# Optimization experiments

Measured on AMD Instinct MI355X. Metric: run time of the kernel, lower is better.

The kernel has to match this reference:

```python
import jax, jax.numpy as jnp
import numpy as np

K = 3       # kernel size
PAD = 1     # k // 2
S = 1       # stride
EPS = 1e-5  # BatchNorm eps


def setup_inputs() -> dict:
    key = jax.random.key(0)
    ks = jax.random.split(key, 7)
    B, C1, C2, H, W = 4, 256, 256, 80, 80
    x = jax.random.normal(ks[0], (B, C1, H, W), dtype=jnp.float32)
    # offset/mask conv params (orig inits these to zero; use small random so
    # the deformable sampling path is actually exercised)
    w_off = jax.random.normal(ks[1], (3 * K * K, C1, K, K), dtype=jnp.float32) * 0.01
    b_off = jax.random.normal(ks[2], (3 * K * K,), dtype=jnp.float32) * 0.01
    weight = jax.random.normal(ks[3], (C2, C1, K, K), dtype=jnp.float32) * 0.05
    bias = jax.random.normal(ks[4], (C2,), dtype=jnp.float32) * 0.05
    gamma = jnp.ones((C2,), dtype=jnp.float32)
    beta = jnp.zeros((C2,), dtype=jnp.float32)
    return {"x": x, "w_off": w_off, "b_off": b_off, "weight": weight,
            "bias": bias, "gamma": gamma, "beta": beta}


def _elastic_head(x, w_off, b_off, weight, bias, gamma, beta):
    B, C, H, W = x.shape
    K2 = K * K
    # offset/mask predictor conv (stride 1, SAME padding -> output H x W)
    off_out = jax.lax.conv_general_dilated(
        x, w_off, (S, S), 'SAME',
        dimension_numbers=('NCHW', 'OIHW', 'NCHW')) + b_off[None, :, None, None]
    o1, o2, m = off_out[:, :K2], off_out[:, K2:2 * K2], off_out[:, 2 * K2:]
    mask = jax.nn.sigmoid(m)                                   # [B,K2,H,W]
    # torchvision layout: channel 2p = dy_p, 2p+1 = dx_p
    off = jnp.concatenate([o1, o2], axis=1).reshape(B, K2, 2, H, W)
    dy, dx = off[:, :, 0], off[:, :, 1]                        # [B,K2,H,W]
    # base sampling grid per kernel tap
    ii, jj = jnp.meshgrid(jnp.arange(K), jnp.arange(K), indexing='ij')
    ii = ii.reshape(K2)
    jj = jj.reshape(K2)
    base_y = (jnp.arange(H)[None, :] * S - PAD + ii[:, None]).astype(x.dtype)  # [K2,H]
    base_x = (jnp.arange(W)[None, :] * S - PAD + jj[:, None]).astype(x.dtype)  # [K2,W]
    ys = dy + base_y[None, :, :, None]                         # [B,K2,H,W]
    xs = dx + base_x[None, :, None, :]
    y0 = jnp.floor(ys)
    x0 = jnp.floor(xs)
    wy = ys - y0
    wx = xs - x0
    y0i = y0.astype(jnp.int32)
    x0i = x0.astype(jnp.int32)
    y1i = y0i + 1
    x1i = x0i + 1
    x_flat = x.reshape(B, C, H * W)

    def gather(yy, xx):
        valid = ((yy >= 0) & (yy < H) & (xx >= 0) & (xx < W)).astype(x.dtype)
        idx = jnp.clip(yy, 0, H - 1) * W + jnp.clip(xx, 0, W - 1)
        g = jax.vmap(lambda xf, ix: xf[:, ix])(x_flat, idx.reshape(B, -1))
        return g.reshape(B, C, K2, H, W) * valid[:, None]

    # bilinear sample with zero padding outside, accumulate corners
    patches = (gather(y0i, x0i) * ((1 - wy) * (1 - wx))[:, None]
               + gather(y0i, x1i) * ((1 - wy) * wx)[:, None]
               + gather(y1i, x0i) * (wy * (1 - wx))[:, None]
               + gather(y1i, x1i) * (wy * wx)[:, None])       # [B,C,K2,H,W]
    patches = patches * mask[:, None]                          # modulation
    # implicit GEMM of deform_conv2d
    out = jnp.einsum('bcphw,ocp->bohw', patches,
                     weight.reshape(weight.shape[0], C, K2)) + bias[None, :, None, None]
    # BatchNorm2d (training-mode batch stats, biased variance) + SiLU
    mean = out.mean(axis=(0, 2, 3))
    var = out.var(axis=(0, 2, 3))
    xn = (out - mean[None, :, None, None]) * jax.lax.rsqrt(var + EPS)[None, :, None, None]
    y_bn = xn * gamma[None, :, None, None] + beta[None, :, None, None]
    return y_bn * jax.nn.sigmoid(y_bn)


def reference(x, w_off, b_off, weight, bias, gamma, beta):
    return _elastic_head(x, w_off, b_off, weight, bias, gamma, beta)
```

## Files before the change

### kernel.cpp

```cpp
#include <hip/hip_runtime.h>
#include <math.h>

constexpr int Hc = 80, Wc = 80, Bn = 4, C1 = 256, C2 = 256;
constexpr int HWn = Hc * Wc;
constexpr int NPIX = Bn * HWn;
constexpr int OFFC = 27;
constexpr int KK   = 2304;

typedef short bf16x8 __attribute__((ext_vector_type(8)));
typedef float f32x4  __attribute__((ext_vector_type(4)));

__device__ __forceinline__ unsigned f2bf(float f) {
    unsigned u = __float_as_uint(f);
    return (u + 0x7FFF + ((u >> 16) & 1)) >> 16;
}

__device__ __forceinline__ unsigned packhi2(float v0, float v1) {
    unsigned h;
    asm("v_cvt_pk_bf16_f32 %0, %1, %2" : "=v"(h) : "v"(v0), "v"(v1));
    return h;
}

__global__ __launch_bounds__(256) void k_wprep(const float* __restrict__ weight,
                                               unsigned short* __restrict__ wB1)
{
    int e = blockIdx.x * 256 + threadIdx.x;
    int kc = e % 40;
    int oc = (e / 40) & 255;
    int s  = e / 10240;
    int p  = s >> 3, cc = s & 7;
    float w = 0.f;
    if (kc < 32) w = weight[((size_t)oc * C1 + cc * 32 + kc) * 9 + p];
    wB1[e] = (unsigned short)f2bf(w);
}

__global__ __launch_bounds__(256) void k_wobprep(const float* __restrict__ w_off,
                                                 unsigned short* __restrict__ wOB)
{
    int e = blockIdx.x * 256 + threadIdx.x;
    int k  = e & 31;
    int oc = (e >> 5) & 31;
    int s  = e >> 10;
    int p  = s >> 3, cc = s & 7;
    float v = 0.f;
    if (oc < 27) v = w_off[((size_t)oc * C1 + cc * 32 + k) * 9 + p];
    wOB[e] = (unsigned short)f2bf(v);
}

__global__ __launch_bounds__(256) void k_xtrans(const float* __restrict__ x,
                                                float* __restrict__ xT,
                                                unsigned short* __restrict__ xTb)
{
    __shared__ float tile[32][33];
    int bid = blockIdx.x;
    int ct  = bid & 7;
    int hwt = (bid >> 3) % 200;
    int b   = bid / 1600;
    int c0  = ct * 32, hw0 = hwt * 32;
    int tid = threadIdx.x;
    int col = tid & 31, rw = tid >> 5;
    const float* xb = x + (size_t)b * C1 * HWn;
    #pragma unroll
    for (int k = 0; k < 4; ++k) {
        int r = rw + k * 8;
        tile[r][col] = xb[(size_t)(c0 + r) * HWn + hw0 + col];
    }
    __syncthreads();
    float* xo = xT + ((size_t)b * HWn + hw0) * C1 + c0;
    unsigned short* xob = xTb + ((size_t)b * HWn + hw0) * C1 + c0;
    #pragma unroll
    for (int k = 0; k < 4; ++k) {
        int r = rw + k * 8;
        float v = tile[col][r];
        xo[(size_t)r * C1 + col]  = v;
        xob[(size_t)r * C1 + col] = (unsigned short)f2bf(v);
    }
}

__global__ __launch_bounds__(256) void k_offmfma(const unsigned short* __restrict__ xTb,
                                                 const unsigned short* __restrict__ wOB,
                                                 const float* __restrict__ b_off,
                                                 float* __restrict__ off)
{
    int t  = threadIdx.x;
    int wv = t >> 6, lane = t & 63;
    int li = lane & 15, kg = lane >> 4;
    int mi = wv & 1;
    int nj = wv >> 1;

    int mtile = ((blockIdx.x & 7) * 100) + (blockIdx.x >> 3);
    int m0  = mtile * 32;
    int b   = m0 / HWn;
    int hw0 = m0 - b * HWn;
    int pxl = hw0 + mi * 16 + li;
    int h = pxl / Wc, w = pxl - h * Wc;

    const unsigned short* xb = xTb + (size_t)b * HWn * C1;

    f32x4 acc = (f32x4){0.f, 0.f, 0.f, 0.f};
    #pragma unroll
    for (int p = 0; p < 9; ++p) {
        int dh = p / 3 - 1, dw = p % 3 - 1;
        int hh = h + dh, ww = w + dw;
        bool valid = (hh >= 0 && hh < Hc && ww >= 0 && ww < Wc);
        int hwp = valid ? (hh * Wc + ww) : 0;
        const unsigned short* arow = xb + (size_t)hwp * C1 + kg * 8;
        const unsigned short* brow = wOB + ((size_t)(p * 8) * 32 + nj * 16 + li) * 32 + kg * 8;
        #pragma unroll
        for (int cc = 0; cc < 8; ++cc) {
            uint4 av = *(const uint4*)(arow + cc * 32);
            if (!valid) av = make_uint4(0, 0, 0, 0);
            uint4 bv = *(const uint4*)(brow + cc * 1024);
            acc = __builtin_amdgcn_mfma_f32_16x16x32_bf16(
                __builtin_bit_cast(bf16x8, av), __builtin_bit_cast(bf16x8, bv), acc, 0, 0, 0);
        }
    }
    int oc = nj * 16 + li;
    if (oc < OFFC) {
        float bs = b_off[oc];
        float4 v;
        v.x = acc[0] + bs; v.y = acc[1] + bs; v.z = acc[2] + bs; v.w = acc[3] + bs;
        int hwd = hw0 + mi * 16 + kg * 4;
        *(float4*)&off[((size_t)b * OFFC + oc) * HWn + hwd] = v;
    }
}

__global__ __launch_bounds__(256) void k_meta(const float* __restrict__ off,
                                              int* __restrict__ crdbuf,
                                              float4* __restrict__ w4buf)
{
    int pair = blockIdx.x * 256 + threadIdx.x;
    int px = pair / 9, p = pair - px * 9;
    int b  = px / HWn, hw = px - b * HWn;
    int h = hw / Wc, w = hw - h * Wc;
    int ii = p / 3, jj = p - ii * 3;

    const float* ob = off + (size_t)b * OFFC * HWn + hw;
    float dy = ob[(2 * p) * HWn];
    float dx = ob[(2 * p + 1) * HWn];
    float mv = ob[(18 + p) * HWn];
    float mask = 1.0f / (1.0f + expf(-mv));
    float ys = dy + (float)(h - 1 + ii);
    float xsv = dx + (float)(w - 1 + jj);
    float y0f = floorf(ys), x0f = floorf(xsv);
    float wy = ys - y0f, wx = xsv - x0f;
    int y0 = (int)y0f, x0 = (int)x0f;
    int y1 = y0 + 1, x1 = x0 + 1;
    float vy0 = (y0 >= 0 && y0 < Hc) ? 1.f : 0.f;
    float vy1 = (y1 >= 0 && y1 < Hc) ? 1.f : 0.f;
    float vx0 = (x0 >= 0 && x0 < Wc) ? 1.f : 0.f;
    float vx1 = (x1 >= 0 && x1 < Wc) ? 1.f : 0.f;
    float4 wv;
    wv.x = mask * (1.f - wy) * (1.f - wx) * vy0 * vx0;
    wv.y = mask * (1.f - wy) * wx         * vy0 * vx1;
    wv.z = mask * wy         * (1.f - wx) * vy1 * vx0;
    wv.w = mask * wy         * wx         * vy1 * vx1;
    int cy0 = min(max(y0, 0), Hc - 1), cy1 = min(max(y1, 0), Hc - 1);
    int cx0 = min(max(x0, 0), Wc - 1), cx1 = min(max(x1, 0), Wc - 1);
    crdbuf[pair] = cy0 | (cy1 << 8) | (cx0 << 16) | (cx1 << 24);
    w4buf[pair]  = wv;
}

__global__ __launch_bounds__(256) void k_gather(const float* __restrict__ xT,
                                                const int* __restrict__ crdbuf,
                                                const float4* __restrict__ w4buf,
                                                unsigned short* __restrict__ Ahi)
{
    int t   = threadIdx.x;
    int wv  = t >> 6, l = t & 63;
    int xcd = blockIdx.x & 7;
    int blk = blockIdx.x >> 3;
    int wgl = (xcd * 100 + blk) * 4 + wv;
    int base = wgl * 72;

    #pragma unroll 2
    for (int i = 0; i < 72; ++i) {
        int pair = base + i;
        int px = pair / 9, p = pair - px * 9;
        int b  = px / HWn;
        int crd = crdbuf[pair];
        float4 w4 = w4buf[pair];
        int cy0 = crd & 255, cy1 = (crd >> 8) & 255;
        int cx0 = (crd >> 16) & 255, cx1 = (crd >> 24) & 255;
        const float* xt = xT + (size_t)b * HWn * C1;
        const float4* g00p = (const float4*)&xt[(size_t)(cy0 * Wc + cx0) * C1];
        const float4* g01p = (const float4*)&xt[(size_t)(cy0 * Wc + cx1) * C1];
        const float4* g10p = (const float4*)&xt[(size_t)(cy1 * Wc + cx0) * C1];
        const float4* g11p = (const float4*)&xt[(size_t)(cy1 * Wc + cx1) * C1];
        float4 g00 = g00p[l], g01 = g01p[l], g10 = g10p[l], g11 = g11p[l];
        float vx = fmaf(w4.x, g00.x, fmaf(w4.y, g01.x, fmaf(w4.z, g10.x, w4.w * g11.x)));
        float vy = fmaf(w4.x, g00.y, fmaf(w4.y, g01.y, fmaf(w4.z, g10.y, w4.w * g11.y)));
        float vz = fmaf(w4.x, g00.z, fmaf(w4.y, g01.z, fmaf(w4.z, g10.z, w4.w * g11.z)));
        float vw = fmaf(w4.x, g00.w, fmaf(w4.y, g01.w, fmaf(w4.z, g10.w, w4.w * g11.w)));
        unsigned h0 = packhi2(vx, vy), h1 = packhi2(vz, vw);
        int s = p * 8 + (l >> 3);
        size_t aidx = ((size_t)s * NPIX + px) * 32 + 4 * (l & 7);
        *(uint2*)&Ahi[aidx] = make_uint2(h0, h1);
    }
}

__global__ __launch_bounds__(256, 4) void k_dmfma(const unsigned short* __restrict__ Ahi,
                                                  const unsigned short* __restrict__ wB1,
                                                  const float* __restrict__ bias,
                                                  float* __restrict__ out)
{
    __shared__ __align__(16) char smem[40960];
    float* Tb = (float*)smem;

    int t  = threadIdx.x;
    int wv = t >> 6, lane = t & 63;
    int li = lane & 15, kg = lane >> 4;
    int mi = wv & 1;
    int nh = wv >> 1;

    int mtile = ((blockIdx.x & 7) * 100) + (blockIdx.x >> 3);
    int m0  = mtile * 32;
    int b   = m0 / HWn;
    int hw0 = m0 - b * HWn;
    int row = m0 + mi * 16 + li;

    auto gllB = [&](int s, int buf) {
        const char* src = (const char*)wB1 + (size_t)s * 20480 + wv * 5120 + lane * 16;
        char* dst = smem + buf * 20480 + wv * 5120;
        #pragma unroll
        for (int i = 0; i < 5; ++i)
            __builtin_amdgcn_global_load_lds(
                (const __attribute__((address_space(1))) void*)(src + i * 1024),
                (__attribute__((address_space(3))) void*)(dst + i * 1024),
                16, 0, 0);
    };
    auto loadA = [&](int s, uint4& hh) {
        size_t base = ((size_t)s * NPIX + row) * 32 + kg * 8;
        hh = *(const uint4*)(Ahi + base);
    };

    f32x4 acc[8];
    #pragma unroll
    for (int n = 0; n < 8; ++n) acc[n] = (f32x4){0.f, 0.f, 0.f, 0.f};

    uint4 a0h, a1h, a2h;
    loadA(0, a0h);
    gllB(0, 0);
    loadA(1, a1h);

    auto step = [&](int s, uint4& ch, uint4& lh) {
        if (s == 71) { asm volatile("s_waitcnt vmcnt(0)" ::: "memory"); }
        else         { asm volatile("s_waitcnt vmcnt(1)" ::: "memory"); }
        __builtin_amdgcn_s_barrier();
        __builtin_amdgcn_sched_barrier(0);
        int cur = s & 1;
        if (s < 71) gllB(s + 1, cur ^ 1);
        __builtin_amdgcn_sched_barrier(0);
        if (s < 70) loadA(s + 2, lh);
        __builtin_amdgcn_sched_barrier(0);
        const unsigned short* Bc = (const unsigned short*)(smem + cur * 20480);
        bf16x8 ah = __builtin_bit_cast(bf16x8, ch);
        __builtin_amdgcn_s_setprio(1);
        #pragma unroll
        for (int nt = 0; nt < 8; ++nt) {
            int oc = nh * 128 + nt * 16 + li;
            bf16x8 bv = *(const bf16x8*)&Bc[oc * 40 + kg * 8];
            acc[nt] = __builtin_amdgcn_mfma_f32_16x16x32_bf16(ah, bv, acc[nt], 0, 0, 0);
        }
        __builtin_amdgcn_s_setprio(0);
    };

    for (int s = 0; s < 72; s += 3) {
        step(s,     a0h, a2h);
        step(s + 1, a1h, a0h);
        step(s + 2, a2h, a1h);
    }

    #pragma unroll
    for (int q = 0; q < 8; ++q) {
        __syncthreads();
        if (nh == (q >> 2)) {
            #pragma unroll
            for (int j = 0; j < 2; ++j) {
                int nt = (q & 3) * 2 + j;
                f32x4 a = acc[nt];
                int rrw = j * 16 + li;
                int col = mi * 16 + kg * 4;
                #pragma unroll
                for (int r = 0; r < 4; ++r)
                    Tb[rrw * 33 + col + r] = a[r];
            }
        }
        __syncthreads();
        int px = t & 31;
        int rw = t >> 5;
        #pragma unroll
        for (int it = 0; it < 4; ++it) {
            int r  = it * 8 + rw;
            int oc = q * 32 + r;
            out[(size_t)(b * C2 + oc) * HWn + hw0 + px] = Tb[r * 33 + px] + bias[oc];
        }
    }
}

__global__ __launch_bounds__(256) void k_bnstats(const float* __restrict__ out,
                                                 float* __restrict__ stats)
{
    int oc = blockIdx.x;
    double s = 0.0, ss = 0.0;
    for (int i = threadIdx.x; i < NPIX; i += 256) {
        int bb = i / HWn;
        int hw = i - bb * HWn;
        float v = out[(size_t)(bb * C2 + oc) * HWn + hw];
        s  += (double)v;
        ss += (double)v * (double)v;
    }
    __shared__ double ls[256], lss[256];
    ls[threadIdx.x] = s; lss[threadIdx.x] = ss;
    __syncthreads();
    for (int st = 128; st > 0; st >>= 1) {
        if (threadIdx.x < st) {
            ls[threadIdx.x]  += ls[threadIdx.x + st];
            lss[threadIdx.x] += lss[threadIdx.x + st];
        }
        __syncthreads();
    }
    if (threadIdx.x == 0) {
        double mean = ls[0] / (double)NPIX;
        double var  = lss[0] / (double)NPIX - mean * mean;
        stats[oc]       = (float)mean;
        stats[256 + oc] = (float)(1.0 / sqrt(var + 1e-5));
    }
}

__global__ __launch_bounds__(256) void k_bnsilu(float* __restrict__ out,
                                                const float* __restrict__ stats,
                                                const float* __restrict__ gamma,
                                                const float* __restrict__ beta)
{
    int n4 = (Bn * C2 * HWn) / 4;
    for (int i = blockIdx.x * blockDim.x + threadIdx.x; i < n4;
         i += gridDim.x * blockDim.x) {
        float4 v = ((float4*)out)[i];
        int e  = i * 4;
        int oc = (e / HWn) & 255;
        float mean = stats[oc];
        float gs   = gamma[oc] * stats[256 + oc];
        float bt   = beta[oc];
        float y;
        y = (v.x - mean) * gs + bt; v.x = y / (1.f + expf(-y));
        y = (v.y - mean) * gs + bt; v.y = y / (1.f + expf(-y));
        y = (v.z - mean) * gs + bt; v.z = y / (1.f + expf(-y));
        y = (v.w - mean) * gs + bt; v.w = y / (1.f + expf(-y));
        ((float4*)out)[i] = v;
    }
}

extern "C" void kernel_launch(void* const* d_in, const int* in_sizes, int n_in,
                              void* d_out, int out_size, void* d_ws, size_t ws_size,
                              hipStream_t stream)
{
    const float* x      = (const float*)d_in[0];
    const float* w_off  = (const float*)d_in[1];
    const float* b_off  = (const float*)d_in[2];
    const float* weight = (const float*)d_in[3];
    const float* bias   = (const float*)d_in[4];
    const float* gamma  = (const float*)d_in[5];
    const float* beta   = (const float*)d_in[6];
    float* out = (float*)d_out;

    char* wsb = (char*)d_ws;
    unsigned short* Ahi  = (unsigned short*)(wsb);
    float*          xT   = (float*)(wsb + 117964800);
    unsigned short* xTb  = (unsigned short*)(wsb + 144179200);
    float*          off  = (float*)(wsb + 157286400);
    unsigned short* wB1  = (unsigned short*)(wsb + 160051200);
    unsigned short* wOB  = (unsigned short*)(wsb + 161525760);
    int*            crdb = (int*)(wsb + 161673216);
    float4*         w4b  = (float4*)(wsb + 162594816);
    float*         stats = (float*)(wsb + 166281216);

    k_wprep    <<<2880, 256, 0, stream>>>(weight, wB1);
    k_wobprep  <<<288, 256, 0, stream>>>(w_off, wOB);
    k_xtrans   <<<6400, 256, 0, stream>>>(x, xT, xTb);
    k_offmfma  <<<800, 256, 0, stream>>>(xTb, wOB, b_off, off);
    k_meta     <<<900, 256, 0, stream>>>(off, crdb, w4b);
    k_gather   <<<800, 256, 0, stream>>>(xT, crdb, w4b, Ahi);
    k_dmfma    <<<800, 256, 0, stream>>>(Ahi, wB1, bias, out);
    k_bnstats  <<<256, 256, 0, stream>>>(out, stats);
    k_bnsilu   <<<2048, 256, 0, stream>>>(out, stats, gamma, beta);
}
```

Before: 250.7 us.

## Retile deform GEMM waves to 2x4 MFMA blocks with unpadded kg-major B layout

Each wave in the main deformable-conv GEMM now computes both 16-row M halves over 64 output channels, instead of one M half over 128 channels. Each B fragment read from LDS now feeds two MFMAs, and each wave issues two A loads per step. The weight prep kernel writes B in a kg-major layout without the 40-element padding, so each K-step's B slice shrinks from 20 KB to 16 KB and LDS use drops. The unpadded layout may cause LDS bank conflicts, and the extra in-flight global loads change the vmcnt accounting.

```diff
diff --git a/kernel.cpp b/kernel.cpp
--- a/kernel.cpp
+++ b/kernel.cpp
@@ -25,12 +25,12 @@
                                                unsigned short* __restrict__ wB1)
 {
     int e = blockIdx.x * 256 + threadIdx.x;
-    int kc = e % 40;
-    int oc = (e / 40) & 255;
-    int s  = e / 10240;
-    int p  = s >> 3, cc = s & 7;
-    float w = 0.f;
-    if (kc < 32) w = weight[((size_t)oc * C1 + cc * 32 + kc) * 9 + p];
+    int kin = e & 7;
+    int oc  = (e >> 3) & 255;
+    int kg  = (e >> 11) & 3;
+    int s   = e >> 13;
+    int p   = s >> 3, cc = s & 7;
+    float w = weight[((size_t)oc * C1 + cc * 32 + kg * 8 + kin) * 9 + p];
     wB1[e] = (unsigned short)f2bf(w);
 }
 
@@ -204,86 +204,93 @@
                                                   const float* __restrict__ bias,
                                                   float* __restrict__ out)
 {
-    __shared__ __align__(16) char smem[40960];
+    __shared__ __align__(16) char smem[32768];
     float* Tb = (float*)smem;
 
     int t  = threadIdx.x;
     int wv = t >> 6, lane = t & 63;
     int li = lane & 15, kg = lane >> 4;
-    int mi = wv & 1;
-    int nh = wv >> 1;
+    int nh = wv;
 
     int mtile = ((blockIdx.x & 7) * 100) + (blockIdx.x >> 3);
     int m0  = mtile * 32;
     int b   = m0 / HWn;
     int hw0 = m0 - b * HWn;
-    int row = m0 + mi * 16 + li;
+    int row0 = m0 + li;
+    int row1 = m0 + 16 + li;
 
     auto gllB = [&](int s, int buf) {
-        const char* src = (const char*)wB1 + (size_t)s * 20480 + wv * 5120 + lane * 16;
-        char* dst = smem + buf * 20480 + wv * 5120;
-        #pragma unroll
-        for (int i = 0; i < 5; ++i)
+        const char* src = (const char*)wB1 + (size_t)s * 16384 + t * 16;
+        char* dst = smem + buf * 16384 + t * 16;
+        #pragma unroll
+        for (int i = 0; i < 4; ++i)
             __builtin_amdgcn_global_load_lds(
-                (const __attribute__((address_space(1))) void*)(src + i * 1024),
-                (__attribute__((address_space(3))) void*)(dst + i * 1024),
+                (const __attribute__((address_space(1))) void*)(src + i * 4096),
+                (__attribute__((address_space(3))) void*)(dst + i * 4096),
                 16, 0, 0);
     };
-    auto loadA = [&](int s, uint4& hh) {
-        size_t base = ((size_t)s * NPIX + row) * 32 + kg * 8;
-        hh = *(const uint4*)(Ahi + base);
+    auto loadA = [&](int s, uint4& h0, uint4& h1) {
+        size_t base = (size_t)s * NPIX * 32 + (size_t)kg * 8;
+        h0 = *(const uint4*)(Ahi + base + (size_t)row0 * 32);
+        h1 = *(const uint4*)(Ahi + base + (size_t)row1 * 32);
     };
 
-    f32x4 acc[8];
-    #pragma unroll
-    for (int n = 0; n < 8; ++n) acc[n] = (f32x4){0.f, 0.f, 0.f, 0.f};
-
-    uint4 a0h, a1h, a2h;
-    loadA(0, a0h);
+    f32x4 acc[2][4];
+    #pragma unroll
+    for (int m = 0; m < 2; ++m)
+        #pragma unroll
+        for (int n = 0; n < 4; ++n) acc[m][n] = (f32x4){0.f, 0.f, 0.f, 0.f};
+
+    uint4 a0m0, a0m1, a1m0, a1m1, a2m0, a2m1;
+    loadA(0, a0m0, a0m1);
     gllB(0, 0);
-    loadA(1, a1h);
-
-    auto step = [&](int s, uint4& ch, uint4& lh) {
+    loadA(1, a1m0, a1m1);
+
+    auto step = [&](int s, uint4& c0, uint4& c1, uint4& l0, uint4& l1) {
         if (s == 71) { asm volatile("s_waitcnt vmcnt(0)" ::: "memory"); }
-        else         { asm volatile("s_waitcnt vmcnt(1)" ::: "memory"); }
+        else         { asm volatile("s_waitcnt vmcnt(2)" ::: "memory"); }
         __builtin_amdgcn_s_barrier();
         __builtin_amdgcn_sched_barrier(0);
         int cur = s & 1;
         if (s < 71) gllB(s + 1, cur ^ 1);
         __builtin_amdgcn_sched_barrier(0);
-        if (s < 70) loadA(s + 2, lh);
+        if (s < 70) loadA(s + 2, l0, l1);
         __builtin_amdgcn_sched_barrier(0);
-        const unsigned short* Bc = (const unsigned short*)(smem + cur * 20480);
-        bf16x8 ah = __builtin_bit_cast(bf16x8, ch);
+        const unsigned short* Bc = (const unsigned short*)(smem + cur * 16384);
+        bf16x8 a0 = __builtin_bit_cast(bf16x8, c0);
+        bf16x8 a1 = __builtin_bit_cast(bf16x8, c1);
         __builtin_amdgcn_s_setprio(1);
         #pragma unroll
-        for (int nt = 0; nt < 8; ++nt) {
-            int oc = nh * 128 + nt * 16 + li;
-            bf16x8 bv = *(const bf16x8*)&Bc[oc * 40 + kg * 8];
-            acc[nt] = __builtin_amdgcn_mfma_f32_16x16x32_bf16(ah, bv, acc[nt], 0, 0, 0);
+        for (int nt = 0; nt < 4; ++nt) {
+            bf16x8 bv = *(const bf16x8*)&Bc[(kg * 256 + nh * 64 + nt * 16 + li) * 8];
+            acc[0][nt] = __builtin_amdgcn_mfma_f32_16x16x32_bf16(a0, bv, acc[0][nt], 0, 0, 0);
+            acc[1][nt] = __builtin_amdgcn_mfma_f32_16x16x32_bf16(a1, bv, acc[1][nt], 0, 0, 0);
         }
         __builtin_amdgcn_s_setprio(0);
     };
 
     for (int s = 0; s < 72; s += 3) {
-        step(s,     a0h, a2h);
-        step(s + 1, a1h, a0h);
-        step(s + 2, a2h, a1h);
+        step(s,     a0m0, a0m1, a2m0, a2m1);
+        step(s + 1, a1m0, a1m1, a0m0, a0m1);
+        step(s + 2, a2m0, a2m1, a1m0, a1m1);
     }
 
     #pragma unroll
     for (int q = 0; q < 8; ++q) {
         __syncthreads();
-        if (nh == (q >> 2)) {
+        if (nh == (q >> 1)) {
             #pragma unroll
-            for (int j = 0; j < 2; ++j) {
-                int nt = (q & 3) * 2 + j;
-                f32x4 a = acc[nt];
-                int rrw = j * 16 + li;
-                int col = mi * 16 + kg * 4;
+            for (int jj = 0; jj < 2; ++jj) {
+                int nt = (q & 1) * 2 + jj;
                 #pragma unroll
-                for (int r = 0; r < 4; ++r)
-                    Tb[rrw * 33 + col + r] = a[r];
+                for (int m = 0; m < 2; ++m) {
+                    f32x4 a = acc[m][nt];
+                    int rrw = jj * 16 + li;
+                    int col = m * 16 + kg * 4;
+                    #pragma unroll
+                    for (int r = 0; r < 4; ++r)
+                        Tb[rrw * 33 + col + r] = a[r];
+                }
             }
         }
         __syncthreads();
@@ -370,12 +377,12 @@
     unsigned short* xTb  = (unsigned short*)(wsb + 144179200);
     float*          off  = (float*)(wsb + 157286400);
     unsigned short* wB1  = (unsigned short*)(wsb + 160051200);
-    unsigned short* wOB  = (unsigned short*)(wsb + 161525760);
-    int*            crdb = (int*)(wsb + 161673216);
-    float4*         w4b  = (float4*)(wsb + 162594816);
-    float*         stats = (float*)(wsb + 166281216);
-
-    k_wprep    <<<2880, 256, 0, stream>>>(weight, wB1);
+    unsigned short* wOB  = (unsigned short*)(wsb + 161230848);
+    int*            crdb = (int*)(wsb + 161378304);
+    float4*         w4b  = (float4*)(wsb + 162299904);
+    float*         stats = (float*)(wsb + 165986304);
+
+    k_wprep    <<<2304, 256, 0, stream>>>(weight, wB1);
     k_wobprep  <<<288, 256, 0, stream>>>(w_off, wOB);
     k_xtrans   <<<6400, 256, 0, stream>>>(x, xT, xTb);
     k_offmfma  <<<800, 256, 0, stream>>>(xTb, wOB, b_off, off);
```

Measured after the change: 253.0 us. Within noise of the previous version (+0.9%).

## Fuse bilinear gather into deformable-conv MFMA kernel, drop im2col buffer

Applied to the files above, without the earlier changes.

Merges the gather kernel and the MFMA GEMM kernel. Each wave now computes its bilinearly sampled bf16 A-fragments in registers straight from xT, so the ~118 MB im2col buffer Ahi is never written to or read back from HBM. Weights are repacked into a layout the MFMA B operand can load directly from global memory, which replaces the double-buffered LDS staging and barriers. In exchange, every block issues scattered gathers with no software pipelining, and B-fragment loads now come from L2 rather than LDS, so latency may be exposed and there may be less overlap with the matrix work.

```diff
diff --git a/kernel.cpp b/kernel.cpp
--- a/kernel.cpp
+++ b/kernel.cpp
@@ -25,12 +25,12 @@
                                                unsigned short* __restrict__ wB1)
 {
     int e = blockIdx.x * 256 + threadIdx.x;
-    int kc = e % 40;
-    int oc = (e / 40) & 255;
-    int s  = e / 10240;
-    int p  = s >> 3, cc = s & 7;
-    float w = 0.f;
-    if (kc < 32) w = weight[((size_t)oc * C1 + cc * 32 + kc) * 9 + p];
+    int kin = e & 7;
+    int oc  = (e >> 3) & 255;
+    int kg  = (e >> 11) & 3;
+    int s   = e >> 13;
+    int p   = s >> 3, cc = s & 7;
+    float w = weight[((size_t)oc * C1 + cc * 32 + kg * 8 + kin) * 9 + p];
     wB1[e] = (unsigned short)f2bf(w);
 }
 
@@ -161,51 +161,14 @@
     w4buf[pair]  = wv;
 }
 
-__global__ __launch_bounds__(256) void k_gather(const float* __restrict__ xT,
+__global__ __launch_bounds__(256) void k_dfused(const float* __restrict__ xT,
                                                 const int* __restrict__ crdbuf,
                                                 const float4* __restrict__ w4buf,
-                                                unsigned short* __restrict__ Ahi)
-{
-    int t   = threadIdx.x;
-    int wv  = t >> 6, l = t & 63;
-    int xcd = blockIdx.x & 7;
-    int blk = blockIdx.x >> 3;
-    int wgl = (xcd * 100 + blk) * 4 + wv;
-    int base = wgl * 72;
-
-    #pragma unroll 2
-    for (int i = 0; i < 72; ++i) {
-        int pair = base + i;
-        int px = pair / 9, p = pair - px * 9;
-        int b  = px / HWn;
-        int crd = crdbuf[pair];
-        float4 w4 = w4buf[pair];
-        int cy0 = crd & 255, cy1 = (crd >> 8) & 255;
-        int cx0 = (crd >> 16) & 255, cx1 = (crd >> 24) & 255;
-        const float* xt = xT + (size_t)b * HWn * C1;
-        const float4* g00p = (const float4*)&xt[(size_t)(cy0 * Wc + cx0) * C1];
-        const float4* g01p = (const float4*)&xt[(size_t)(cy0 * Wc + cx1) * C1];
-        const float4* g10p = (const float4*)&xt[(size_t)(cy1 * Wc + cx0) * C1];
-        const float4* g11p = (const float4*)&xt[(size_t)(cy1 * Wc + cx1) * C1];
-        float4 g00 = g00p[l], g01 = g01p[l], g10 = g10p[l], g11 = g11p[l];
-        float vx = fmaf(w4.x, g00.x, fmaf(w4.y, g01.x, fmaf(w4.z, g10.x, w4.w * g11.x)));
-        float vy = fmaf(w4.x, g00.y, fmaf(w4.y, g01.y, fmaf(w4.z, g10.y, w4.w * g11.y)));
-        float vz = fmaf(w4.x, g00.z, fmaf(w4.y, g01.z, fmaf(w4.z, g10.z, w4.w * g11.z)));
-        float vw = fmaf(w4.x, g00.w, fmaf(w4.y, g01.w, fmaf(w4.z, g10.w, w4.w * g11.w)));
-        unsigned h0 = packhi2(vx, vy), h1 = packhi2(vz, vw);
-        int s = p * 8 + (l >> 3);
-        size_t aidx = ((size_t)s * NPIX + px) * 32 + 4 * (l & 7);
-        *(uint2*)&Ahi[aidx] = make_uint2(h0, h1);
-    }
-}
-
-__global__ __launch_bounds__(256, 4) void k_dmfma(const unsigned short* __restrict__ Ahi,
-                                                  const unsigned short* __restrict__ wB1,
-                                                  const float* __restrict__ bias,
-                                                  float* __restrict__ out)
-{
-    __shared__ __align__(16) char smem[40960];
-    float* Tb = (float*)smem;
+                                                const unsigned short* __restrict__ wB1,
+                                                const float* __restrict__ bias,
+                                                float* __restrict__ out)
+{
+    __shared__ float Tb[32 * 33];
 
     int t  = threadIdx.x;
     int wv = t >> 6, lane = t & 63;
@@ -217,58 +180,57 @@
     int m0  = mtile * 32;
     int b   = m0 / HWn;
     int hw0 = m0 - b * HWn;
-    int row = m0 + mi * 16 + li;
-
-    auto gllB = [&](int s, int buf) {
-        const char* src = (const char*)wB1 + (size_t)s * 20480 + wv * 5120 + lane * 16;
-        char* dst = smem + buf * 20480 + wv * 5120;
+    int px  = m0 + mi * 16 + li;
+
+    const float* xtb = xT + (size_t)b * HWn * C1;
+
+    f32x4 acc[8];
+    #pragma unroll
+    for (int n = 0; n < 8; ++n) acc[n] = (f32x4){0.f, 0.f, 0.f, 0.f};
+
+    #pragma unroll 1
+    for (int p = 0; p < 9; ++p) {
+        int pair = px * 9 + p;
+        int crd = crdbuf[pair];
+        float4 w4 = w4buf[pair];
+        int cy0 = crd & 255, cy1 = (crd >> 8) & 255;
+        int cx0 = (crd >> 16) & 255, cx1 = (crd >> 24) & 255;
+        const float* c00 = &xtb[(size_t)(cy0 * Wc + cx0) * C1 + kg * 8];
+        const float* c01 = &xtb[(size_t)(cy0 * Wc + cx1) * C1 + kg * 8];
+        const float* c10 = &xtb[(size_t)(cy1 * Wc + cx0) * C1 + kg * 8];
+        const float* c11 = &xtb[(size_t)(cy1 * Wc + cx1) * C1 + kg * 8];
         #pragma unroll
-        for (int i = 0; i < 5; ++i)
-            __builtin_amdgcn_global_load_lds(
-                (const __attribute__((address_space(1))) void*)(src + i * 1024),
-                (__attribute__((address_space(3))) void*)(dst + i * 1024),
-                16, 0, 0);
-    };
-    auto loadA = [&](int s, uint4& hh) {
-        size_t base = ((size_t)s * NPIX + row) * 32 + kg * 8;
-        hh = *(const uint4*)(Ahi + base);
-    };
-
-    f32x4 acc[8];
-    #pragma unroll
-    for (int n = 0; n < 8; ++n) acc[n] = (f32x4){0.f, 0.f, 0.f, 0.f};
-
-    uint4 a0h, a1h, a2h;
-    loadA(0, a0h);
-    gllB(0, 0);
-    loadA(1, a1h);
-
-    auto step = [&](int s, uint4& ch, uint4& lh) {
-        if (s == 71) { asm volatile("s_waitcnt vmcnt(0)" ::: "memory"); }
-        else         { asm volatile("s_waitcnt vmcnt(1)" ::: "memory"); }
-        __builtin_amdgcn_s_barrier();
-        __builtin_amdgcn_sched_barrier(0);
-        int cur = s & 1;
-        if (s < 71) gllB(s + 1, cur ^ 1);
-        __builtin_amdgcn_sched_barrier(0);
-        if (s < 70) loadA(s + 2, lh);
-        __builtin_amdgcn_sched_barrier(0);
-        const unsigned short* Bc = (const unsigned short*)(smem + cur * 20480);
-        bf16x8 ah = __builtin_bit_cast(bf16x8, ch);
-        __builtin_amdgcn_s_setprio(1);
-        #pragma unroll
-        for (int nt = 0; nt < 8; ++nt) {
-            int oc = nh * 128 + nt * 16 + li;
-            bf16x8 bv = *(const bf16x8*)&Bc[oc * 40 + kg * 8];
-            acc[nt] = __builtin_amdgcn_mfma_f32_16x16x32_bf16(ah, bv, acc[nt], 0, 0, 0);
-        }
-        __builtin_amdgcn_s_setprio(0);
-    };
-
-    for (int s = 0; s < 72; s += 3) {
-        step(s,     a0h, a2h);
-        step(s + 1, a1h, a0h);
-        step(s + 2, a2h, a1h);
+        for (int cc = 0; cc < 8; ++cc) {
+            int s = p * 8 + cc;
+            float4 a0 = *(const float4*)(c00 + cc * 32);
+            float4 a1 = *(const float4*)(c00 + cc * 32 + 4);
+            float4 b0 = *(const float4*)(c01 + cc * 32);
+            float4 b1 = *(const float4*)(c01 + cc * 32 + 4);
+            float4 d0 = *(const float4*)(c10 + cc * 32);
+            float4 d1 = *(const float4*)(c10 + cc * 32 + 4);
+            float4 e0 = *(const float4*)(c11 + cc * 32);
+            float4 e1 = *(const float4*)(c11 + cc * 32 + 4);
+            float v[8];
+            v[0] = fmaf(w4.x, a0.x, fmaf(w4.y, b0.x, fmaf(w4.z, d0.x, w4.w * e0.x)));
+            v[1] = fmaf(w4.x, a0.y, fmaf(w4.y, b0.y, fmaf(w4.z, d0.y, w4.w * e0.y)));
+            v[2] = fmaf(w4.x, a0.z, fmaf(w4.y, b0.z, fmaf(w4.z, d0.z, w4.w * e0.z)));
+            v[3] = fmaf(w4.x, a0.w, fmaf(w4.y, b0.w, fmaf(w4.z, d0.w, w4.w * e0.w)));
+            v[4] = fmaf(w4.x, a1.x, fmaf(w4.y, b1.x, fmaf(w4.z, d1.x, w4.w * e1.x)));
+            v[5] = fmaf(w4.x, a1.y, fmaf(w4.y, b1.y, fmaf(w4.z, d1.y, w4.w * e1.y)));
+            v[6] = fmaf(w4.x, a1.z, fmaf(w4.y, b1.z, fmaf(w4.z, d1.z, w4.w * e1.z)));
+            v[7] = fmaf(w4.x, a1.w, fmaf(w4.y, b1.w, fmaf(w4.z, d1.w, w4.w * e1.w)));
+            unsigned h0 = packhi2(v[0], v[1]);
+            unsigned h1 = packhi2(v[2], v[3]);
+            unsigned h2 = packhi2(v[4], v[5]);
+            unsigned h3 = packhi2(v[6], v[7]);
+            bf16x8 av = __builtin_bit_cast(bf16x8, make_uint4(h0, h1, h2, h3));
+            const unsigned short* bq = wB1 + ((size_t)(s * 4 + kg) * 256 + nh * 128 + li) * 8;
+            #pragma unroll
+            for (int nt = 0; nt < 8; ++nt) {
+                bf16x8 bv = *(const bf16x8*)(bq + nt * 128);
+                acc[nt] = __builtin_amdgcn_mfma_f32_16x16x32_bf16(av, bv, acc[nt], 0, 0, 0);
+            }
+        }
     }
 
     #pragma unroll
@@ -279,21 +241,21 @@
             for (int j = 0; j < 2; ++j) {
                 int nt = (q & 3) * 2 + j;
                 f32x4 a = acc[nt];
-                int rrw = j * 16 + li;
+                int row = j * 16 + li;
                 int col = mi * 16 + kg * 4;
                 #pragma unroll
                 for (int r = 0; r < 4; ++r)
-                    Tb[rrw * 33 + col + r] = a[r];
+                    Tb[row * 33 + col + r] = a[r];
             }
         }
         __syncthreads();
-        int px = t & 31;
+        int pxs = t & 31;
         int rw = t >> 5;
         #pragma unroll
         for (int it = 0; it < 4; ++it) {
             int r  = it * 8 + rw;
             int oc = q * 32 + r;
-            out[(size_t)(b * C2 + oc) * HWn + hw0 + px] = Tb[r * 33 + px] + bias[oc];
+            out[(size_t)(b * C2 + oc) * HWn + hw0 + pxs] = Tb[r * 33 + pxs] + bias[oc];
         }
     }
 }
@@ -365,23 +327,21 @@
     float* out = (float*)d_out;
 
     char* wsb = (char*)d_ws;
-    unsigned short* Ahi  = (unsigned short*)(wsb);
-    float*          xT   = (float*)(wsb + 117964800);
-    unsigned short* xTb  = (unsigned short*)(wsb + 144179200);
-    float*          off  = (float*)(wsb + 157286400);
-    unsigned short* wB1  = (unsigned short*)(wsb + 160051200);
-    unsigned short* wOB  = (unsigned short*)(wsb + 161525760);
-    int*            crdb = (int*)(wsb + 161673216);
-    float4*         w4b  = (float4*)(wsb + 162594816);
-    float*         stats = (float*)(wsb + 166281216);
-
-    k_wprep    <<<2880, 256, 0, stream>>>(weight, wB1);
+    float*          xT   = (float*)(wsb);
+    unsigned short* xTb  = (unsigned short*)(wsb + 26214400);
+    float*          off  = (float*)(wsb + 39321600);
+    unsigned short* wB1  = (unsigned short*)(wsb + 42086400);
+    unsigned short* wOB  = (unsigned short*)(wsb + 43266048);
+    int*            crdb = (int*)(wsb + 43413504);
+    float4*         w4b  = (float4*)(wsb + 44335104);
+    float*         stats = (float*)(wsb + 48021504);
+
+    k_wprep    <<<2304, 256, 0, stream>>>(weight, wB1);
     k_wobprep  <<<288, 256, 0, stream>>>(w_off, wOB);
     k_xtrans   <<<6400, 256, 0, stream>>>(x, xT, xTb);
     k_offmfma  <<<800, 256, 0, stream>>>(xTb, wOB, b_off, off);
     k_meta     <<<900, 256, 0, stream>>>(off, crdb, w4b);
-    k_gather   <<<800, 256, 0, stream>>>(xT, crdb, w4b, Ahi);
-    k_dmfma    <<<800, 256, 0, stream>>>(Ahi, wB1, bias, out);
+    k_dfused   <<<800, 256, 0, stream>>>(xT, crdb, w4b, wB1, bias, out);
     k_bnstats  <<<256, 256, 0, stream>>>(out, stats);
     k_bnsilu   <<<2048, 256, 0, stream>>>(out, stats, gamma, beta);
 }
```

New measurement: 446.4 us. 78.0% more time.
